# Optimization experiments

Hardware: AMD Instinct MI355X
Metric: run time of the kernel (lower is better)

Reference implementation:

```python
import jax, jax.numpy as jnp
import numpy as np

PI = float(np.pi)


def _cgs(node_feats, node_centre, nbr_idx, graph_w,
         mean_rho, mean_theta, prec_rho, prec_theta, conv_w, use_graph_weights):
    # node_feats: [B,N,C]; node_centre: [B,N,2]; nbr_idx: [B,N,K] (within-sample node ids)
    # graph_w: [B*N*K, 1] or None; mean/prec: [1,R]; conv_w: [R, C, OUT//R]
    B, N, C = node_feats.shape
    K = nbr_idx.shape[-1]
    R = mean_rho.shape[-1]
    BN = B * N
    # flat neighbor index into B*N nodes (coords[1])
    flat_nbr = (jnp.arange(B, dtype=nbr_idx.dtype)[:, None, None] * N + nbr_idx).reshape(BN * K)
    src = jnp.repeat(jnp.arange(BN), K)
    centre = node_centre.reshape(BN, 2)
    d = centre[src] - centre[flat_nbr]                    # [E,2], node_intersect 'minus'
    rho = jnp.sqrt(d[:, 0] ** 2 + d[:, 1] ** 2)
    theta = jnp.arctan2(d[:, 0], d[:, 1])
    # gaussian mixture edge weights over R kernels
    w_rho = jnp.exp(-0.5 * (rho[:, None] - mean_rho) ** 2 / (1e-14 + prec_rho ** 2))
    first_angle = jnp.abs(theta[:, None] - mean_theta)
    second_angle = jnp.abs(2.0 * PI - first_angle)
    w_theta = jnp.exp(-0.5 * jnp.minimum(first_angle, second_angle) ** 2
                      / (1e-14 + prec_theta ** 2))
    w = w_rho * w_theta
    w = jnp.where(jnp.isnan(w), 0.0, w)
    w = w / jnp.sum(w, axis=1, keepdims=True)             # [E,R]
    if use_graph_weights:
        w = graph_w * w
    ew = w.reshape(BN, K, R)
    nj = node_feats.reshape(BN, C)[flat_nbr].reshape(BN, K, C)   # gather neighbors
    agg = jnp.einsum('ekr,ekc->erc', ew, nj).reshape(B, N, R, C)  # weighted bmm
    out = jnp.einsum('bnrc,rcd->bnrd', agg, conv_w).reshape(B, N, R * conv_w.shape[-1])
    return jax.nn.relu(out)


def setup_inputs() -> dict:
    key = jax.random.key(0)
    ks = jax.random.split(key, 16)
    B, N, K, C, R, OUT = 64, 100, 16, 1024, 8, 1024
    D = OUT // R
    return {
        "node_feats": jax.random.normal(ks[0], (B, N, C), jnp.float32),
        "node_centre": jax.random.uniform(ks[1], (B, N, 2), dtype=jnp.float32),
        "graph_w": jax.random.uniform(ks[2], (B * N * K, 1), dtype=jnp.float32),
        "nbr_idx": jax.random.randint(ks[3], (B, N, K), 0, N, dtype=jnp.int32),
        "mean_rho1": jax.random.uniform(ks[4], (1, R), dtype=jnp.float32),
        "mean_theta1": jax.random.uniform(ks[5], (1, R), dtype=jnp.float32, minval=-PI, maxval=PI),
        "prec_rho1": jax.random.uniform(ks[6], (1, R), dtype=jnp.float32),
        "prec_theta1": jax.random.uniform(ks[7], (1, R), dtype=jnp.float32),
        "conv_w1": jax.random.normal(ks[8], (R, C, D), jnp.float32) * 0.02,
        "mean_rho2": jax.random.uniform(ks[9], (1, R), dtype=jnp.float32),
        "mean_theta2": jax.random.uniform(ks[10], (1, R), dtype=jnp.float32, minval=-PI, maxval=PI),
        "prec_rho2": jax.random.uniform(ks[11], (1, R), dtype=jnp.float32),
        "prec_theta2": jax.random.uniform(ks[12], (1, R), dtype=jnp.float32),
        "conv_w2": jax.random.normal(ks[13], (R, OUT, D), jnp.float32) * 0.02,
    }


def reference(node_feats, node_centre, graph_w,
              mean_rho1, mean_theta1, prec_rho1, prec_theta1, conv_w1,
              mean_rho2, mean_theta2, prec_rho2, prec_theta2, conv_w2,
              nbr_idx):
    # NodeFeatLayer('cgs_sum^8') = Sequential(CgsNodeFeat(use_graph_weights=True),
    #                                          CgsNodeFeat(use_graph_weights=False))
    h = _cgs(node_feats, node_centre, nbr_idx, graph_w,
             mean_rho1, mean_theta1, prec_rho1, prec_theta1, conv_w1, True)
    h = _cgs(h, node_centre, nbr_idx, None,
             mean_rho2, mean_theta2, prec_rho2, prec_theta2, conv_w2, False)
    return h
```

## Files before the change

kernel.cpp:

```cpp
#include <hip/hip_runtime.h>
#include <hip/hip_bf16.h>
#include <math.h>

#define B_   64
#define N_   100
#define K_   16
#define C_   1024
#define R_   8
#define BN_  6400
#define E_   102400

typedef __attribute__((ext_vector_type(8))) short bf16x8;
typedef __attribute__((ext_vector_type(4))) float f32x4;

__device__ __forceinline__ float bf2f(ushort h) {
    union { uint32_t u; float f; } v; v.u = ((uint32_t)h) << 16; return v.f;
}
__device__ __forceinline__ ushort f2bf(float f) {
    union { float f; uint32_t u; } v; v.f = f;
    uint32_t r = v.u + 0x7FFFu + ((v.u >> 16) & 1u);
    return (ushort)(r >> 16);
}

__device__ __forceinline__ void gload_lds16(const void* g, void* l) {
    __builtin_amdgcn_global_load_lds(
        (const __attribute__((address_space(1))) void*)g,
        (__attribute__((address_space(3))) void*)l, 16, 0, 0);
}

__global__ __launch_bounds__(256) void edge_weights_kernel(
        const float* __restrict__ centre, const int* __restrict__ nbr_idx,
        const float* __restrict__ graph_w,
        const float* __restrict__ mr1, const float* __restrict__ mt1,
        const float* __restrict__ pr1, const float* __restrict__ pt1,
        const float* __restrict__ mr2, const float* __restrict__ mt2,
        const float* __restrict__ pr2, const float* __restrict__ pt2,
        float* __restrict__ w1, float* __restrict__ w2) {
    int e = blockIdx.x * blockDim.x + threadIdx.x;
    if (e >= E_) return;
    int n = e / K_;
    int b = n / N_;
    int fn = b * N_ + nbr_idx[e];
    float dx = centre[2*n]   - centre[2*fn];
    float dy = centre[2*n+1] - centre[2*fn+1];
    float rho   = sqrtf(dx*dx + dy*dy);
    float theta = atan2f(dx, dy);
    const float TWO_PI = 6.28318530717958647692f;
    {
        float w[R_]; float s = 0.f;
        #pragma unroll
        for (int r = 0; r < R_; ++r) {
            float dr = rho - mr1[r];
            float wr = expf(-0.5f * dr * dr / (1e-14f + pr1[r]*pr1[r]));
            float fa = fabsf(theta - mt1[r]);
            float mi = fminf(fa, fabsf(TWO_PI - fa));
            float wt = expf(-0.5f * mi * mi / (1e-14f + pt1[r]*pt1[r]));
            float ww = wr * wt;
            if (isnan(ww)) ww = 0.f;
            w[r] = ww; s += ww;
        }
        float gw = graph_w[e];
        #pragma unroll
        for (int r = 0; r < R_; ++r) w1[e*R_ + r] = gw * (w[r] / s);
    }
    {
        float w[R_]; float s = 0.f;
        #pragma unroll
        for (int r = 0; r < R_; ++r) {
            float dr = rho - mr2[r];
            float wr = expf(-0.5f * dr * dr / (1e-14f + pr2[r]*pr2[r]));
            float fa = fabsf(theta - mt2[r]);
            float mi = fminf(fa, fabsf(TWO_PI - fa));
            float wt = expf(-0.5f * mi * mi / (1e-14f + pt2[r]*pt2[r]));
            float ww = wr * wt;
            if (isnan(ww)) ww = 0.f;
            w[r] = ww; s += ww;
        }
        #pragma unroll
        for (int r = 0; r < R_; ++r) w2[e*R_ + r] = w[r] / s;
    }
}

__global__ __launch_bounds__(256) void cast_x_kernel(
        const float* __restrict__ X, ushort* __restrict__ Xb) {
    int i = (blockIdx.x * 256 + threadIdx.x) * 4;
    float4 v = *(const float4*)&X[i];
    ushort4 o; o.x = f2bf(v.x); o.y = f2bf(v.y); o.z = f2bf(v.z); o.w = f2bf(v.w);
    *(ushort4*)&Xb[i] = o;
}

__global__ __launch_bounds__(256) void wtrans_kernel(
        const float* __restrict__ W, ushort* __restrict__ Wt) {
    int j = blockIdx.x;
    int c = blockIdx.y * 256 + threadIdx.x;
    float v = W[((j >> 7) << 17) + c * 128 + (j & 127)];
    Wt[j * 1024 + c] = f2bf(v);
}

__global__ __launch_bounds__(256) void gemm_bf16_kernel(
        const ushort* __restrict__ Xb,
        const ushort* __restrict__ Wt,
        ushort* __restrict__ P) {
    __shared__ ushort As[128][32];
    __shared__ ushort Bs[128][32];
    int tile = blockIdx.x;
    int swz  = (tile & 7) * 50 + (tile >> 3);
    int m0 = (swz >> 3) * 128, n0 = (swz & 7) * 128;
    int t = threadIdx.x, wid = t >> 6, lane = t & 63;
    int wr = wid >> 1, wc = wid & 1;

    int srow  = lane >> 2;
    int sslot = (lane & 3) ^ ((lane >> 2) & 3) ^ (lane >> 4);
    int pslot = (lane >> 4) ^ (lane & 3) ^ ((lane >> 2) & 3);

    f32x4 acc[4][4];
    #pragma unroll
    for (int i = 0; i < 4; ++i)
        #pragma unroll
        for (int j = 0; j < 4; ++j) acc[i][j] = (f32x4)0.f;

    int arow = wr * 64 + (lane & 15);
    int brow = wc * 64 + (lane & 15);

    for (int c0 = 0; c0 < 1024; c0 += 32) {
        #pragma unroll
        for (int q = 0; q < 2; ++q) {
            int rowblk = (q * 4 + wid) * 16;
            gload_lds16(Xb + (size_t)(m0 + rowblk + srow) * 1024 + c0 + sslot * 8,
                        &As[rowblk][0]);
            gload_lds16(Wt + (size_t)(n0 + rowblk + srow) * 1024 + c0 + sslot * 8,
                        &Bs[rowblk][0]);
        }
        __syncthreads();
        bf16x8 af[4], bfr[4];
        #pragma unroll
        for (int mi = 0; mi < 4; ++mi)
            af[mi] = *(const bf16x8*)&As[arow + mi * 16][pslot * 8];
        #pragma unroll
        for (int ni = 0; ni < 4; ++ni)
            bfr[ni] = *(const bf16x8*)&Bs[brow + ni * 16][pslot * 8];
        #pragma unroll
        for (int mi = 0; mi < 4; ++mi)
            #pragma unroll
            for (int ni = 0; ni < 4; ++ni)
                acc[mi][ni] = __builtin_amdgcn_mfma_f32_16x16x32_bf16(
                    af[mi], bfr[ni], acc[mi][ni], 0, 0, 0);
        __syncthreads();
    }
    int col = lane & 15, rq = lane >> 4;
    #pragma unroll
    for (int mi = 0; mi < 4; ++mi) {
        int row = m0 + wr * 64 + mi * 16 + rq * 4;
        #pragma unroll
        for (int ni = 0; ni < 4; ++ni) {
            int cc = n0 + wc * 64 + ni * 16 + col;
            #pragma unroll
            for (int q = 0; q < 4; ++q)
                P[(size_t)(row + q) * 1024 + cc] = f2bf(acc[mi][ni][q]);
        }
    }
}

__global__ __launch_bounds__(256) void aggregate_kernel(
        const ushort* __restrict__ P, const float* __restrict__ w,
        const int* __restrict__ nbr_idx,
        ushort* __restrict__ outB, float* __restrict__ outF) {
    __shared__ float wv[K_][R_];
    __shared__ int fnbr[K_];
    int bid = blockIdx.x;
    int n = (bid & 7) * 800 + (bid >> 3);
    int t = threadIdx.x;
    if (t < K_ * R_) { int k = t >> 3, r = t & 7; wv[k][r] = w[(n * K_ + k) * R_ + r]; }
    if (t < K_) fnbr[t] = (n / N_) * N_ + nbr_idx[n * K_ + t];
    __syncthreads();
    int j0 = t * 4;
    int r = t >> 5;
    float a0 = 0.f, a1 = 0.f, a2 = 0.f, a3 = 0.f;
    #pragma unroll
    for (int k = 0; k < K_; ++k) {
        ushort4 v = *(const ushort4*)&P[(size_t)fnbr[k] * 1024 + j0];
        float wk = wv[k][r];
        a0 += wk * bf2f(v.x); a1 += wk * bf2f(v.y);
        a2 += wk * bf2f(v.z); a3 += wk * bf2f(v.w);
    }
    a0 = fmaxf(a0, 0.f); a1 = fmaxf(a1, 0.f);
    a2 = fmaxf(a2, 0.f); a3 = fmaxf(a3, 0.f);
    if (outB) {
        ushort4 o; o.x = f2bf(a0); o.y = f2bf(a1); o.z = f2bf(a2); o.w = f2bf(a3);
        *(ushort4*)&outB[(size_t)n * 1024 + j0] = o;
    } else {
        float4 o; o.x = a0; o.y = a1; o.z = a2; o.w = a3;
        *(float4*)&outF[(size_t)n * 1024 + j0] = o;
    }
}

extern "C" void kernel_launch(void* const* d_in, const int* in_sizes, int n_in,
                              void* d_out, int out_size, void* d_ws, size_t ws_size,
                              hipStream_t stream) {
    const float* node_feats = (const float*)d_in[0];
    const float* centre     = (const float*)d_in[1];
    const float* graph_w    = (const float*)d_in[2];
    const int*   nbr_idx    = (const int*)  d_in[3];
    const float* mr1 = (const float*)d_in[4];
    const float* mt1 = (const float*)d_in[5];
    const float* pr1 = (const float*)d_in[6];
    const float* pt1 = (const float*)d_in[7];
    const float* cw1 = (const float*)d_in[8];
    const float* mr2 = (const float*)d_in[9];
    const float* mt2 = (const float*)d_in[10];
    const float* pr2 = (const float*)d_in[11];
    const float* pt2 = (const float*)d_in[12];
    const float* cw2 = (const float*)d_in[13];

    char* ws = (char*)d_ws;
    float*  w1  = (float*)ws;                 ws += (size_t)E_ * R_ * 4;
    float*  w2  = (float*)ws;                 ws += (size_t)E_ * R_ * 4;
    ushort* Xb  = (ushort*)ws;                ws += (size_t)BN_ * 1024 * 2;
    ushort* W1t = (ushort*)ws;                ws += (size_t)1024 * 1024 * 2;
    ushort* W2t = (ushort*)ws;                ws += (size_t)1024 * 1024 * 2;
    ushort* hb  = (ushort*)ws;                ws += (size_t)BN_ * 1024 * 2;
    ushort* P   = (ushort*)ws;

    float* out = (float*)d_out;

    edge_weights_kernel<<<(E_ + 255) / 256, 256, 0, stream>>>(
        centre, nbr_idx, graph_w, mr1, mt1, pr1, pt1, mr2, mt2, pr2, pt2, w1, w2);
    cast_x_kernel<<<BN_ * 1024 / 4 / 256, 256, 0, stream>>>(node_feats, Xb);
    wtrans_kernel<<<dim3(1024, 4), 256, 0, stream>>>(cw1, W1t);
    wtrans_kernel<<<dim3(1024, 4), 256, 0, stream>>>(cw2, W2t);

    gemm_bf16_kernel<<<400, 256, 0, stream>>>(Xb, W1t, P);
    aggregate_kernel<<<BN_, 256, 0, stream>>>(P, w1, nbr_idx, hb, nullptr);

    gemm_bf16_kernel<<<400, 256, 0, stream>>>(hb, W2t, P);
    aggregate_kernel<<<BN_, 256, 0, stream>>>(P, w2, nbr_idx, nullptr, out);
}
```

Before: 201.6 us.

## Double-buffer GEMM LDS, tile weight transpose, widen aggregate and weight stores

The bf16 GEMM now double-buffers its A/B LDS tiles, so the next K-slice is fetched while MFMAs run on the current one. The two weight-transpose launches become one LDS-tiled launch that reads and writes coalesced rows. The aggregate kernel handles two nodes per block with 8-wide bf16 loads and stores, and the edge-weight kernel writes its results as float4 vectors. The cost is double the GEMM LDS footprint, which may reduce occupancy, and fewer, heavier aggregate blocks.

```diff
diff --git a/kernel.cpp b/kernel.cpp
--- a/kernel.cpp
+++ b/kernel.cpp
@@ -60,8 +60,10 @@
             w[r] = ww; s += ww;
         }
         float gw = graph_w[e];
-        #pragma unroll
-        for (int r = 0; r < R_; ++r) w1[e*R_ + r] = gw * (w[r] / s);
+        float4 o0 = { gw*(w[0]/s), gw*(w[1]/s), gw*(w[2]/s), gw*(w[3]/s) };
+        float4 o1 = { gw*(w[4]/s), gw*(w[5]/s), gw*(w[6]/s), gw*(w[7]/s) };
+        *(float4*)&w1[e*R_]     = o0;
+        *(float4*)&w1[e*R_ + 4] = o1;
     }
     {
         float w[R_]; float s = 0.f;
@@ -76,8 +78,10 @@
             if (isnan(ww)) ww = 0.f;
             w[r] = ww; s += ww;
         }
-        #pragma unroll
-        for (int r = 0; r < R_; ++r) w2[e*R_ + r] = w[r] / s;
+        float4 o0 = { w[0]/s, w[1]/s, w[2]/s, w[3]/s };
+        float4 o1 = { w[4]/s, w[5]/s, w[6]/s, w[7]/s };
+        *(float4*)&w2[e*R_]     = o0;
+        *(float4*)&w2[e*R_ + 4] = o1;
     }
 }
 
@@ -90,19 +94,38 @@
 }
 
 __global__ __launch_bounds__(256) void wtrans_kernel(
-        const float* __restrict__ W, ushort* __restrict__ Wt) {
-    int j = blockIdx.x;
-    int c = blockIdx.y * 256 + threadIdx.x;
-    float v = W[((j >> 7) << 17) + c * 128 + (j & 127)];
-    Wt[j * 1024 + c] = f2bf(v);
+        const float* __restrict__ W1, ushort* __restrict__ Wt1,
+        const float* __restrict__ W2, ushort* __restrict__ Wt2) {
+    __shared__ ushort T[64][138];
+    const float* W = (blockIdx.z == 0) ? W1 : W2;
+    ushort*    Wt = (blockIdx.z == 0) ? Wt1 : Wt2;
+    int r  = blockIdx.y;
+    int c0 = blockIdx.x * 64;
+    int t  = threadIdx.x;
+    int lane6 = t & 63;
+    #pragma unroll
+    for (int it = 0; it < 16; ++it) {
+        int ch = (t >> 6) + 4 * it;
+        int d  = lane6 * 2;
+        const float* src = &W[(((size_t)r << 10) + c0 + ch) * 128 + d];
+        float2 v = *(const float2*)src;
+        T[ch][d]     = f2bf(v.x);
+        T[ch][d + 1] = f2bf(v.y);
+    }
+    __syncthreads();
+    #pragma unroll
+    for (int it = 0; it < 32; ++it) {
+        int d = (t >> 6) + 4 * it;
+        Wt[(size_t)(r * 128 + d) * 1024 + c0 + lane6] = T[lane6][d];
+    }
 }
 
 __global__ __launch_bounds__(256) void gemm_bf16_kernel(
         const ushort* __restrict__ Xb,
         const ushort* __restrict__ Wt,
         ushort* __restrict__ P) {
-    __shared__ ushort As[128][32];
-    __shared__ ushort Bs[128][32];
+    __shared__ ushort As[2][128][32];
+    __shared__ ushort Bs[2][128][32];
     int tile = blockIdx.x;
     int swz  = (tile & 7) * 50 + (tile >> 3);
     int m0 = (swz >> 3) * 128, n0 = (swz & 7) * 128;
@@ -121,24 +144,32 @@
 
     int arow = wr * 64 + (lane & 15);
     int brow = wc * 64 + (lane & 15);
-
-    for (int c0 = 0; c0 < 1024; c0 += 32) {
-        #pragma unroll
-        for (int q = 0; q < 2; ++q) {
-            int rowblk = (q * 4 + wid) * 16;
-            gload_lds16(Xb + (size_t)(m0 + rowblk + srow) * 1024 + c0 + sslot * 8,
-                        &As[rowblk][0]);
-            gload_lds16(Wt + (size_t)(n0 + rowblk + srow) * 1024 + c0 + sslot * 8,
-                        &Bs[rowblk][0]);
-        }
-        __syncthreads();
+    int rowblk0 = wid * 16, rowblk1 = (4 + wid) * 16;
+    const ushort* agp = Xb + (size_t)(m0 + srow) * 1024 + sslot * 8;
+    const ushort* bgp = Wt + (size_t)(n0 + srow) * 1024 + sslot * 8;
+
+    gload_lds16(agp + (size_t)rowblk0 * 1024, &As[0][rowblk0][0]);
+    gload_lds16(bgp + (size_t)rowblk0 * 1024, &Bs[0][rowblk0][0]);
+    gload_lds16(agp + (size_t)rowblk1 * 1024, &As[0][rowblk1][0]);
+    gload_lds16(bgp + (size_t)rowblk1 * 1024, &Bs[0][rowblk1][0]);
+    __syncthreads();
+
+    for (int ts = 0; ts < 32; ++ts) {
+        int cur = ts & 1;
+        if (ts < 31) {
+            int c1 = (ts + 1) * 32;
+            gload_lds16(agp + (size_t)rowblk0 * 1024 + c1, &As[cur ^ 1][rowblk0][0]);
+            gload_lds16(bgp + (size_t)rowblk0 * 1024 + c1, &Bs[cur ^ 1][rowblk0][0]);
+            gload_lds16(agp + (size_t)rowblk1 * 1024 + c1, &As[cur ^ 1][rowblk1][0]);
+            gload_lds16(bgp + (size_t)rowblk1 * 1024 + c1, &Bs[cur ^ 1][rowblk1][0]);
+        }
         bf16x8 af[4], bfr[4];
         #pragma unroll
         for (int mi = 0; mi < 4; ++mi)
-            af[mi] = *(const bf16x8*)&As[arow + mi * 16][pslot * 8];
+            af[mi] = *(const bf16x8*)&As[cur][arow + mi * 16][pslot * 8];
         #pragma unroll
         for (int ni = 0; ni < 4; ++ni)
-            bfr[ni] = *(const bf16x8*)&Bs[brow + ni * 16][pslot * 8];
+            bfr[ni] = *(const bf16x8*)&Bs[cur][brow + ni * 16][pslot * 8];
         #pragma unroll
         for (int mi = 0; mi < 4; ++mi)
             #pragma unroll
@@ -165,32 +196,44 @@
         const ushort* __restrict__ P, const float* __restrict__ w,
         const int* __restrict__ nbr_idx,
         ushort* __restrict__ outB, float* __restrict__ outF) {
-    __shared__ float wv[K_][R_];
-    __shared__ int fnbr[K_];
+    __shared__ float wv[2][K_][R_];
+    __shared__ int fnbr[2][K_];
     int bid = blockIdx.x;
-    int n = (bid & 7) * 800 + (bid >> 3);
+    int n0 = ((bid & 7) * 400 + (bid >> 3)) * 2;
     int t = threadIdx.x;
-    if (t < K_ * R_) { int k = t >> 3, r = t & 7; wv[k][r] = w[(n * K_ + k) * R_ + r]; }
-    if (t < K_) fnbr[t] = (n / N_) * N_ + nbr_idx[n * K_ + t];
+    {
+        int node = t >> 7, rem = t & 127, k = rem >> 3, r = rem & 7;
+        wv[node][k][r] = w[((size_t)(n0 + node) * K_ + k) * R_ + r];
+    }
+    if (t < 32) {
+        int node = t >> 4, k = t & 15, nn = n0 + node;
+        fnbr[node][k] = (nn / N_) * N_ + nbr_idx[nn * K_ + k];
+    }
     __syncthreads();
-    int j0 = t * 4;
-    int r = t >> 5;
-    float a0 = 0.f, a1 = 0.f, a2 = 0.f, a3 = 0.f;
+    int node = t >> 7, jj = t & 127;
+    int j0 = jj * 8;
+    int r  = jj >> 4;
+    float a[8] = {};
     #pragma unroll
     for (int k = 0; k < K_; ++k) {
-        ushort4 v = *(const ushort4*)&P[(size_t)fnbr[k] * 1024 + j0];
-        float wk = wv[k][r];
-        a0 += wk * bf2f(v.x); a1 += wk * bf2f(v.y);
-        a2 += wk * bf2f(v.z); a3 += wk * bf2f(v.w);
-    }
-    a0 = fmaxf(a0, 0.f); a1 = fmaxf(a1, 0.f);
-    a2 = fmaxf(a2, 0.f); a3 = fmaxf(a3, 0.f);
+        bf16x8 v = *(const bf16x8*)&P[(size_t)fnbr[node][k] * 1024 + j0];
+        float wk = wv[node][k][r];
+        #pragma unroll
+        for (int q = 0; q < 8; ++q) a[q] += wk * bf2f((ushort)v[q]);
+    }
+    #pragma unroll
+    for (int q = 0; q < 8; ++q) a[q] = fmaxf(a[q], 0.f);
+    size_t base = (size_t)(n0 + node) * 1024 + j0;
     if (outB) {
-        ushort4 o; o.x = f2bf(a0); o.y = f2bf(a1); o.z = f2bf(a2); o.w = f2bf(a3);
-        *(ushort4*)&outB[(size_t)n * 1024 + j0] = o;
+        bf16x8 o;
+        #pragma unroll
+        for (int q = 0; q < 8; ++q) o[q] = (short)f2bf(a[q]);
+        *(bf16x8*)&outB[base] = o;
     } else {
-        float4 o; o.x = a0; o.y = a1; o.z = a2; o.w = a3;
-        *(float4*)&outF[(size_t)n * 1024 + j0] = o;
+        float4 o0 = { a[0], a[1], a[2], a[3] };
+        float4 o1 = { a[4], a[5], a[6], a[7] };
+        *(float4*)&outF[base]     = o0;
+        *(float4*)&outF[base + 4] = o1;
     }
 }
 
@@ -226,12 +269,11 @@
     edge_weights_kernel<<<(E_ + 255) / 256, 256, 0, stream>>>(
         centre, nbr_idx, graph_w, mr1, mt1, pr1, pt1, mr2, mt2, pr2, pt2, w1, w2);
     cast_x_kernel<<<BN_ * 1024 / 4 / 256, 256, 0, stream>>>(node_feats, Xb);
-    wtrans_kernel<<<dim3(1024, 4), 256, 0, stream>>>(cw1, W1t);
-    wtrans_kernel<<<dim3(1024, 4), 256, 0, stream>>>(cw2, W2t);
+    wtrans_kernel<<<dim3(16, 8, 2), 256, 0, stream>>>(cw1, W1t, cw2, W2t);
 
     gemm_bf16_kernel<<<400, 256, 0, stream>>>(Xb, W1t, P);
-    aggregate_kernel<<<BN_, 256, 0, stream>>>(P, w1, nbr_idx, hb, nullptr);
+    aggregate_kernel<<<BN_ / 2, 256, 0, stream>>>(P, w1, nbr_idx, hb, nullptr);
 
     gemm_bf16_kernel<<<400, 256, 0, stream>>>(hb, W2t, P);
-    aggregate_kernel<<<BN_, 256, 0, stream>>>(P, w2, nbr_idx, nullptr, out);
-}
+    aggregate_kernel<<<BN_ / 2, 256, 0, stream>>>(P, w2, nbr_idx, nullptr, out);
+}
```

Result: faster. 192.5 us (-4.5%).
